# Performance work log

Measured on AMD Instinct MI355X. Metric: run time of the kernel, lower is better.

The kernel has to match this reference:

```python
import jax, jax.numpy as jnp
import numpy as np

D_MODEL = 1024
N_HEADS = 16
MAX_LAG = 512
D_K = D_MODEL // N_HEADS


def setup_inputs() -> dict:
    key = jax.random.key(0)
    ks = jax.random.split(key, 11)
    B, S = 2, 2048
    x = jax.random.normal(ks[0], (B, S, D_MODEL), dtype=jnp.float32)
    lag = jax.random.randint(ks[1], (S,), 0, MAX_LAG + 1, dtype=jnp.int64)
    scale = 1.0 / np.sqrt(D_MODEL)
    wq = jax.random.normal(ks[2], (D_MODEL, D_MODEL), dtype=jnp.float32) * scale
    bq = jnp.zeros((D_MODEL,), dtype=jnp.float32)
    wk = jax.random.normal(ks[3], (D_MODEL, D_MODEL), dtype=jnp.float32) * scale
    bk = jnp.zeros((D_MODEL,), dtype=jnp.float32)
    wv = jax.random.normal(ks[4], (D_MODEL, D_MODEL), dtype=jnp.float32) * scale
    bv = jnp.zeros((D_MODEL,), dtype=jnp.float32)
    wo = jax.random.normal(ks[5], (D_MODEL, D_MODEL), dtype=jnp.float32) * scale
    bo = jnp.zeros((D_MODEL,), dtype=jnp.float32)
    lag_bias = jax.random.normal(ks[6], (N_HEADS, MAX_LAG + 1), dtype=jnp.float32) * 0.02
    return {"x": x, "lag": lag, "wq": wq, "bq": bq, "wk": wk, "bk": bk,
            "wv": wv, "bv": bv, "wo": wo, "bo": bo, "lag_bias": lag_bias}


def reference(x, lag, wq, bq, wk, bk, wv, bv, wo, bo, lag_bias):
    B, S, D = x.shape
    H, dk = N_HEADS, D_K
    # projections: torch Linear is x @ W.T + b; here weights stored as (in, out)
    q = (x @ wq + bq).reshape(B, S, H, dk).transpose(0, 2, 1, 3)  # (B,H,S,dk)
    k = (x @ wk + bk).reshape(B, S, H, dk).transpose(0, 2, 1, 3)
    v = (x @ wv + bv).reshape(B, S, H, dk).transpose(0, 2, 1, 3)
    scores = jnp.einsum('bhqd,bhkd->bhqk', q, k) / jnp.sqrt(jnp.float32(dk))
    ld = jnp.abs(lag[:, None] - lag[None, :]).astype(jnp.int32)  # (S,S)
    bias = lag_bias[:, ld]  # (H,S,S)
    attn = jax.nn.softmax(scores + bias[None], axis=-1)
    out = jnp.einsum('bhqk,bhkd->bhqd', attn, v)
    out = out.transpose(0, 2, 1, 3).reshape(B, S, D)
    return out @ wo + bo
```

## Files before the change

### kernel.cpp

```cpp
#include <hip/hip_runtime.h>

typedef __bf16 bf16;
typedef __bf16 bf16x8 __attribute__((ext_vector_type(8)));
typedef float f32x4 __attribute__((ext_vector_type(4)));

__device__ __forceinline__ f32x4 mfma16(bf16x8 a, bf16x8 b, f32x4 c) {
  return __builtin_amdgcn_mfma_f32_16x16x32_bf16(a, b, c, 0, 0, 0);
}
__device__ __forceinline__ void gload16(const bf16* g, bf16* l) {
  __builtin_amdgcn_global_load_lds((const __attribute__((address_space(1))) unsigned int*)g,
                                   (__attribute__((address_space(3))) unsigned int*)l, 16, 0, 0);
}

__global__ __launch_bounds__(256) void cvt_x_kernel(const float* __restrict__ in,
                                                    bf16* __restrict__ out, int n8) {
  int i = blockIdx.x * 256 + threadIdx.x;
  if (i >= n8) return;
  const float4* p = (const float4*)in + (size_t)i * 2;
  float4 f0 = p[0], f1 = p[1];
  bf16x8 o;
  o[0] = (bf16)f0.x; o[1] = (bf16)f0.y; o[2] = (bf16)f0.z; o[3] = (bf16)f0.w;
  o[4] = (bf16)f1.x; o[5] = (bf16)f1.y; o[6] = (bf16)f1.z; o[7] = (bf16)f1.w;
  *((bf16x8*)out + i) = o;
}

__global__ __launch_bounds__(256) void cvt_wt_kernel(const float* __restrict__ in,
                                                     bf16* __restrict__ out) {
  __shared__ float t[64][68];
  int bx = blockIdx.x & 15;
  int by = blockIdx.x >> 4;
  int tid = threadIdx.x;
  int r = tid >> 2, p = tid & 3;
  const float* src = in + (size_t)(by * 64 + r) * 1024 + bx * 64 + p * 16;
#pragma unroll
  for (int j = 0; j < 16; j += 4)
    *(float4*)&t[r][p * 16 + j] = *(const float4*)(src + j);
  __syncthreads();
  int n = tid >> 2, sp = tid & 3;
  bf16 tmp[16];
#pragma unroll
  for (int j = 0; j < 16; ++j) tmp[j] = (bf16)t[sp * 16 + j][n];
  bf16* dst = out + (size_t)(bx * 64 + n) * 1024 + by * 64 + sp * 16;
  *(bf16x8*)dst = *(bf16x8*)&tmp[0];
  *(bf16x8*)(dst + 8) = *(bf16x8*)&tmp[8];
}

__global__ void cvt_bias_kernel(const float* __restrict__ bq, const float* __restrict__ bk,
                                const float* __restrict__ bv, float* __restrict__ out) {
  int i = blockIdx.x * 256 + threadIdx.x;
  if (i < 1024) out[i] = bq[i];
  else if (i < 2048) out[i] = bk[i - 1024];
  else if (i < 3072) out[i] = bv[i - 2048];
}

template <int OUT_BF16>
__global__ __launch_bounds__(256) void gemm_bt_kernel(
    const bf16* __restrict__ A, const bf16* __restrict__ Bt,
    const float* __restrict__ bias, void* __restrict__ C,
    int M, int N, int K, int scale_cols, float scale_val) {
  __shared__ __align__(16) bf16 As[128 * 64];
  __shared__ __align__(16) bf16 Bs[128 * 64];
  int bn = blockIdx.x * 128, bm = blockIdx.y * 128;
  int tid = threadIdx.x;
  int l = tid & 63;
  int w = tid >> 6;
  int wr = w >> 1, wc = w & 1;
  int g = l >> 4, c = l & 15;
  int swz = (c & 7) << 3;

  int srow = l >> 3;
  int scol = ((l & 7) ^ srow) << 3;
  const bf16* Ap = A + (size_t)(bm + w * 32 + srow) * K + scol;
  const bf16* Bp = Bt + (size_t)(bn + w * 32 + srow) * K + scol;
  bf16* AsW = As + w * 32 * 64;
  bf16* BsW = Bs + w * 32 * 64;

  f32x4 acc[4][4] = {};
  for (int k0 = 0; k0 < K; k0 += 64) {
    __syncthreads();
#pragma unroll
    for (int i = 0; i < 4; ++i) {
      gload16(Ap + (size_t)(8 * i) * K + k0, AsW + i * 512);
      gload16(Bp + (size_t)(8 * i) * K + k0, BsW + i * 512);
    }
    __syncthreads();
#pragma unroll
    for (int kh = 0; kh < 2; ++kh) {
      bf16x8 af[4], bfr[4];
#pragma unroll
      for (int m = 0; m < 4; ++m)
        af[m] = *(const bf16x8*)&As[(wr * 64 + m * 16 + c) * 64 + ((kh * 32 + g * 8) ^ swz)];
#pragma unroll
      for (int n = 0; n < 4; ++n)
        bfr[n] = *(const bf16x8*)&Bs[(wc * 64 + n * 16 + c) * 64 + ((kh * 32 + g * 8) ^ swz)];
#pragma unroll
      for (int m = 0; m < 4; ++m)
#pragma unroll
        for (int n = 0; n < 4; ++n)
          acc[m][n] = mfma16(af[m], bfr[n], acc[m][n]);
    }
  }
  int rowb = bm + wr * 64;
  int colb = bn + wc * 64;
#pragma unroll
  for (int n = 0; n < 4; ++n) {
    int col = colb + n * 16 + c;
    float bv = bias[col];
    float s = (col < scale_cols) ? scale_val : 1.0f;
#pragma unroll
    for (int m = 0; m < 4; ++m) {
      int row = rowb + m * 16 + g * 4;
#pragma unroll
      for (int j = 0; j < 4; ++j) {
        float v = (acc[m][n][j] + bv) * s;
        if (OUT_BF16)
          ((bf16*)C)[(size_t)(row + j) * N + col] = (bf16)v;
        else
          ((float*)C)[(size_t)(row + j) * N + col] = v;
      }
    }
  }
}

__global__ __launch_bounds__(256) void transpose_v_kernel(const bf16* __restrict__ qkv,
                                                          bf16* __restrict__ vt) {
  __shared__ bf16 t[64][72];
  int blk = blockIdx.x;
  int st = blk & 31;
  int h = (blk >> 5) & 15;
  int b = blk >> 9;
  int tid = threadIdx.x;
  int r = tid >> 2, p = tid & 3;
  const bf16* src = qkv + (size_t)(b * 2048 + st * 64 + r) * 3072 + 2048 + h * 64 + p * 16;
  *(bf16x8*)&t[r][p * 16] = *(const bf16x8*)src;
  *(bf16x8*)&t[r][p * 16 + 8] = *(const bf16x8*)(src + 8);
  __syncthreads();
  int d = tid >> 2, sp = tid & 3;
  bf16 tmp[16];
#pragma unroll
  for (int j = 0; j < 16; ++j) tmp[j] = t[sp * 16 + j][d];
  bf16* dst = vt + (size_t)((b * 16 + h) * 64 + d) * 2048 + st * 64 + sp * 16;
  *(bf16x8*)dst = *(bf16x8*)&tmp[0];
  *(bf16x8*)(dst + 8) = *(bf16x8*)&tmp[8];
}

__global__ __launch_bounds__(256) void attn_kernel(
    const bf16* __restrict__ qkv, const bf16* __restrict__ vt,
    const int* __restrict__ lag, const float* __restrict__ lag_bias,
    bf16* __restrict__ out) {
  __shared__ __align__(16) bf16 Ks0[64 * 64];
  __shared__ __align__(16) bf16 Vs0[64 * 64];
  __shared__ __align__(16) bf16 Ks1[64 * 64];
  __shared__ __align__(16) bf16 Vs1[64 * 64];
  __shared__ __align__(16) bf16 Ps[4][32][72];
  __shared__ float bias_s[516];
  __shared__ int lag_s[2048];

  int blk = blockIdx.x;
  blk = (blk & 7) * 64 + (blk >> 3);
  int qt = blk & 15;
  int h = (blk >> 4) & 15;
  int b = blk >> 8;
  int tid = threadIdx.x;
  int w = tid >> 6, l = tid & 63, g = l >> 4, c = l & 15;

  for (int i = tid; i < 513; i += 256) bias_s[i] = lag_bias[h * 513 + i] * 1.44269504f;
  for (int i = tid; i < 2048; i += 256) lag_s[i] = lag[i];

  int q0 = qt * 128 + w * 32;
  const bf16* qbase = qkv + (size_t)(b * 2048 + q0) * 3072 + h * 64;
  bf16x8 qf[2][2];
#pragma unroll
  for (int m = 0; m < 2; ++m)
#pragma unroll
    for (int kh = 0; kh < 2; ++kh)
      qf[m][kh] = *(const bf16x8*)(qbase + (size_t)(m * 16 + c) * 3072 + kh * 32 + g * 8);

  int swz = (c & 7) << 3;
  int off0 = (g * 8) ^ swz;
  int off1 = off0 ^ 32;

  int r0 = w * 16 + (l >> 3);
  int colE = ((l & 7) ^ (l >> 3)) << 3;
  const bf16* kbase = qkv + (size_t)(b * 2048) * 3072 + 1024 + h * 64;
  const bf16* vbase = vt + (size_t)(b * 16 + h) * 64 * 2048;
  const bf16* kg0 = kbase + (size_t)r0 * 3072 + colE;
  const bf16* kg1 = kbase + (size_t)(r0 + 8) * 3072 + colE;
  const bf16* vg0 = vbase + (size_t)r0 * 2048 + colE;
  const bf16* vg1 = vbase + (size_t)(r0 + 8) * 2048 + colE;

#define STAGE(KD, VD)                    \
  do {                                   \
    gload16(kg0, KD + w * 1024);         \
    gload16(kg1, KD + w * 1024 + 512);   \
    gload16(vg0, VD + w * 1024);         \
    gload16(vg1, VD + w * 1024 + 512);   \
    kg0 += 64 * 3072; kg1 += 64 * 3072;  \
    vg0 += 64; vg1 += 64;                \
  } while (0)

  STAGE(Ks0, Vs0);
  __syncthreads();

  int lagq[2][4];
#pragma unroll
  for (int m = 0; m < 2; ++m)
#pragma unroll
    for (int j = 0; j < 4; ++j) lagq[m][j] = lag_s[q0 + m * 16 + g * 4 + j];

  f32x4 oacc[2][4] = {};
  float psum[2][4] = {};

#define TILE(KB, VB, KT)                                                          \
  do {                                                                            \
    f32x4 sf[2][4] = {};                                                          \
    int lagk[4];                                                                  \
    __builtin_amdgcn_s_setprio(1);                                                \
    _Pragma("unroll") for (int kb = 0; kb < 4; ++kb) {                            \
      int row = kb * 16 + c;                                                      \
      bf16x8 k0 = *(const bf16x8*)&KB[row * 64 + off0];                           \
      bf16x8 k1 = *(const bf16x8*)&KB[row * 64 + off1];                           \
      sf[0][kb] = mfma16(qf[0][0], k0, sf[0][kb]);                                \
      sf[0][kb] = mfma16(qf[0][1], k1, sf[0][kb]);                                \
      sf[1][kb] = mfma16(qf[1][0], k0, sf[1][kb]);                                \
      sf[1][kb] = mfma16(qf[1][1], k1, sf[1][kb]);                                \
      lagk[kb] = lag_s[(KT) + kb * 16 + c];                                       \
    }                                                                             \
    __builtin_amdgcn_s_setprio(0);                                                \
    _Pragma("unroll") for (int m = 0; m < 2; ++m)                                 \
    _Pragma("unroll") for (int kb = 0; kb < 4; ++kb)                              \
    _Pragma("unroll") for (int j = 0; j < 4; ++j) {                               \
      int ld = lagq[m][j] - lagk[kb];                                             \
      ld = ld < 0 ? -ld : ld;                                                     \
      float p = __builtin_amdgcn_exp2f(sf[m][kb][j] + bias_s[ld]);                \
      psum[m][j] += p;                                                            \
      Ps[w][m * 16 + g * 4 + j][kb * 16 + c] = (bf16)p;                           \
    }                                                                             \
    asm volatile("s_waitcnt lgkmcnt(0)" ::: "memory");                            \
    __builtin_amdgcn_s_setprio(1);                                                \
    _Pragma("unroll") for (int ph = 0; ph < 2; ++ph) {                            \
      bf16x8 pa0 = *(const bf16x8*)&Ps[w][c][ph * 32 + g * 8];                    \
      bf16x8 pa1 = *(const bf16x8*)&Ps[w][16 + c][ph * 32 + g * 8];               \
      int voff = ph ? off1 : off0;                                                \
      _Pragma("unroll") for (int n = 0; n < 4; ++n) {                             \
        bf16x8 vf = *(const bf16x8*)&VB[(n * 16 + c) * 64 + voff];                \
        oacc[0][n] = mfma16(pa0, vf, oacc[0][n]);                                 \
        oacc[1][n] = mfma16(pa1, vf, oacc[1][n]);                                 \
      }                                                                           \
    }                                                                             \
    __builtin_amdgcn_s_setprio(0);                                                \
  } while (0)

  for (int kt = 0; kt < 2048; kt += 128) {
    if (kt + 64 < 2048) STAGE(Ks1, Vs1);
    TILE(Ks0, Vs0, kt);
    __syncthreads();
    if (kt + 128 < 2048) STAGE(Ks0, Vs0);
    TILE(Ks1, Vs1, kt + 64);
    __syncthreads();
  }

#pragma unroll
  for (int m = 0; m < 2; ++m) {
#pragma unroll
    for (int j = 0; j < 4; ++j) {
      float s = psum[m][j];
      s += __shfl_xor(s, 1);
      s += __shfl_xor(s, 2);
      s += __shfl_xor(s, 4);
      s += __shfl_xor(s, 8);
      float inv = 1.f / s;
      bf16* ob = out + (size_t)(b * 2048 + q0 + m * 16 + g * 4 + j) * 1024 + h * 64;
#pragma unroll
      for (int n = 0; n < 4; ++n)
        ob[n * 16 + c] = (bf16)(oacc[m][n][j] * inv);
    }
  }
#undef STAGE
#undef TILE
}

extern "C" void kernel_launch(void* const* d_in, const int* in_sizes, int n_in,
                              void* d_out, int out_size, void* d_ws, size_t ws_size,
                              hipStream_t stream) {
  const float* x        = (const float*)d_in[0];
  const int*   lag      = (const int*)d_in[1];
  const float* wq       = (const float*)d_in[2];
  const float* bq       = (const float*)d_in[3];
  const float* wk       = (const float*)d_in[4];
  const float* bk       = (const float*)d_in[5];
  const float* wv       = (const float*)d_in[6];
  const float* bv       = (const float*)d_in[7];
  const float* wo       = (const float*)d_in[8];
  const float* bo       = (const float*)d_in[9];
  const float* lag_bias = (const float*)d_in[10];

  char* ws = (char*)d_ws;
  bf16*  xb    = (bf16*)ws;
  bf16*  wqkvt = (bf16*)(ws + (8u  << 20));
  bf16*  wot   = (bf16*)(ws + (14u << 20));
  float* bqkv  = (float*)(ws + (16u << 20));
  bf16*  qkv   = (bf16*)(ws + (17u << 20));
  bf16*  vtb   = (bf16*)(ws + (41u << 20));
  bf16*  aout  = (bf16*)(ws + (49u << 20));

  cvt_x_kernel<<<2048, 256, 0, stream>>>(x, xb, 524288);
  cvt_wt_kernel<<<256, 256, 0, stream>>>(wq, wqkvt);
  cvt_wt_kernel<<<256, 256, 0, stream>>>(wk, wqkvt + (1u << 20));
  cvt_wt_kernel<<<256, 256, 0, stream>>>(wv, wqkvt + (2u << 20));
  cvt_wt_kernel<<<256, 256, 0, stream>>>(wo, wot);
  cvt_bias_kernel<<<12, 256, 0, stream>>>(bq, bk, bv, bqkv);
  gemm_bt_kernel<1><<<dim3(24, 32), 256, 0, stream>>>(
      xb, wqkvt, bqkv, qkv, 4096, 3072, 1024, 1024, 0.125f * 1.44269504f);
  transpose_v_kernel<<<1024, 256, 0, stream>>>(qkv, vtb);
  attn_kernel<<<512, 256, 0, stream>>>(qkv, vtb, lag, lag_bias, aout);
  gemm_bt_kernel<0><<<dim3(8, 32), 256, 0, stream>>>(
      aout, wot, bo, (float*)d_out, 4096, 1024, 1024, 0, 1.0f);
}
```

Measured before the change: 170.8 us.

## Permute keys by sorted lag and pack K contiguously for attention

Adds a single-block counting sort of the lag vector that produces a permutation and the sorted lag values. K is gathered in that order into a contiguous per-head buffer, and V is transposed in the same order, so attention reads K as dense 64-wide rows instead of 3072-strided rows. The sorted lags make bias lookups within a key tile more local. The sort runs on one block with a serial prefix and a scan per lag value, and the extra pack kernel adds a pass over K. The s_setprio hints inside the attention tile are also removed.

```diff
diff --git a/kernel.cpp b/kernel.cpp
--- a/kernel.cpp
+++ b/kernel.cpp
@@ -53,6 +53,45 @@
   else if (i < 3072) out[i] = bv[i - 2048];
 }
 
+__global__ __launch_bounds__(512) void sort_lag_kernel(const int* __restrict__ lag,
+                                                       int* __restrict__ perm,
+                                                       int* __restrict__ slag) {
+  __shared__ int l[2048];
+  __shared__ int cnt[513];
+  __shared__ int pre[513];
+  int tid = threadIdx.x;
+  for (int i = tid; i < 2048; i += 512) l[i] = lag[i];
+  for (int i = tid; i < 513; i += 512) cnt[i] = 0;
+  __syncthreads();
+  for (int i = tid; i < 2048; i += 512) atomicAdd(&cnt[l[i]], 1);
+  __syncthreads();
+  if (tid == 0) {
+    int a = 0;
+    for (int v = 0; v < 513; ++v) { pre[v] = a; a += cnt[v]; }
+  }
+  __syncthreads();
+  for (int v = tid; v < 513; v += 512) {
+    int base = pre[v];
+    for (int j = 0; j < 2048; ++j) {
+      if (l[j] == v) { perm[base] = j; slag[base] = v; ++base; }
+    }
+  }
+}
+
+__global__ __launch_bounds__(256) void pack_k_kernel(const bf16* __restrict__ qkv,
+                                                     const int* __restrict__ perm,
+                                                     bf16* __restrict__ kp) {
+  int blk = blockIdx.x;
+  int st = blk & 31, h = (blk >> 5) & 15, b = blk >> 9;
+  int tid = threadIdx.x;
+  int r = tid >> 2, p = tid & 3;
+  int src_s = perm[st * 64 + r];
+  const bf16* src = qkv + (size_t)(b * 2048 + src_s) * 3072 + 1024 + h * 64 + p * 16;
+  bf16* dst = kp + (size_t)((b * 16 + h) * 2048 + st * 64 + r) * 64 + p * 16;
+  *(bf16x8*)dst = *(const bf16x8*)src;
+  *(bf16x8*)(dst + 8) = *(const bf16x8*)(src + 8);
+}
+
 template <int OUT_BF16>
 __global__ __launch_bounds__(256) void gemm_bt_kernel(
     const bf16* __restrict__ A, const bf16* __restrict__ Bt,
@@ -123,6 +162,7 @@
 }
 
 __global__ __launch_bounds__(256) void transpose_v_kernel(const bf16* __restrict__ qkv,
+                                                          const int* __restrict__ perm,
                                                           bf16* __restrict__ vt) {
   __shared__ bf16 t[64][72];
   int blk = blockIdx.x;
@@ -131,7 +171,8 @@
   int b = blk >> 9;
   int tid = threadIdx.x;
   int r = tid >> 2, p = tid & 3;
-  const bf16* src = qkv + (size_t)(b * 2048 + st * 64 + r) * 3072 + 2048 + h * 64 + p * 16;
+  int src_s = perm[st * 64 + r];
+  const bf16* src = qkv + (size_t)(b * 2048 + src_s) * 3072 + 2048 + h * 64 + p * 16;
   *(bf16x8*)&t[r][p * 16] = *(const bf16x8*)src;
   *(bf16x8*)&t[r][p * 16 + 8] = *(const bf16x8*)(src + 8);
   __syncthreads();
@@ -145,8 +186,9 @@
 }
 
 __global__ __launch_bounds__(256) void attn_kernel(
-    const bf16* __restrict__ qkv, const bf16* __restrict__ vt,
-    const int* __restrict__ lag, const float* __restrict__ lag_bias,
+    const bf16* __restrict__ qkv, const bf16* __restrict__ kp,
+    const bf16* __restrict__ vt, const int* __restrict__ lag,
+    const int* __restrict__ slag, const float* __restrict__ lag_bias,
     bf16* __restrict__ out) {
   __shared__ __align__(16) bf16 Ks0[64 * 64];
   __shared__ __align__(16) bf16 Vs0[64 * 64];
@@ -165,7 +207,7 @@
   int w = tid >> 6, l = tid & 63, g = l >> 4, c = l & 15;
 
   for (int i = tid; i < 513; i += 256) bias_s[i] = lag_bias[h * 513 + i] * 1.44269504f;
-  for (int i = tid; i < 2048; i += 256) lag_s[i] = lag[i];
+  for (int i = tid; i < 2048; i += 256) lag_s[i] = slag[i];
 
   int q0 = qt * 128 + w * 32;
   const bf16* qbase = qkv + (size_t)(b * 2048 + q0) * 3072 + h * 64;
@@ -176,16 +218,22 @@
     for (int kh = 0; kh < 2; ++kh)
       qf[m][kh] = *(const bf16x8*)(qbase + (size_t)(m * 16 + c) * 3072 + kh * 32 + g * 8);
 
+  int lagq[2][4];
+#pragma unroll
+  for (int m = 0; m < 2; ++m)
+#pragma unroll
+    for (int j = 0; j < 4; ++j) lagq[m][j] = lag[q0 + m * 16 + g * 4 + j];
+
   int swz = (c & 7) << 3;
   int off0 = (g * 8) ^ swz;
   int off1 = off0 ^ 32;
 
   int r0 = w * 16 + (l >> 3);
   int colE = ((l & 7) ^ (l >> 3)) << 3;
-  const bf16* kbase = qkv + (size_t)(b * 2048) * 3072 + 1024 + h * 64;
+  const bf16* kbase = kp + (size_t)(b * 16 + h) * 2048 * 64;
   const bf16* vbase = vt + (size_t)(b * 16 + h) * 64 * 2048;
-  const bf16* kg0 = kbase + (size_t)r0 * 3072 + colE;
-  const bf16* kg1 = kbase + (size_t)(r0 + 8) * 3072 + colE;
+  const bf16* kg0 = kbase + (size_t)r0 * 64 + colE;
+  const bf16* kg1 = kbase + (size_t)(r0 + 8) * 64 + colE;
   const bf16* vg0 = vbase + (size_t)r0 * 2048 + colE;
   const bf16* vg1 = vbase + (size_t)(r0 + 8) * 2048 + colE;
 
@@ -195,18 +243,12 @@
     gload16(kg1, KD + w * 1024 + 512);   \
     gload16(vg0, VD + w * 1024);         \
     gload16(vg1, VD + w * 1024 + 512);   \
-    kg0 += 64 * 3072; kg1 += 64 * 3072;  \
+    kg0 += 64 * 64; kg1 += 64 * 64;      \
     vg0 += 64; vg1 += 64;                \
   } while (0)
 
   STAGE(Ks0, Vs0);
   __syncthreads();
-
-  int lagq[2][4];
-#pragma unroll
-  for (int m = 0; m < 2; ++m)
-#pragma unroll
-    for (int j = 0; j < 4; ++j) lagq[m][j] = lag_s[q0 + m * 16 + g * 4 + j];
 
   f32x4 oacc[2][4] = {};
   float psum[2][4] = {};
@@ -215,7 +257,6 @@
   do {                                                                            \
     f32x4 sf[2][4] = {};                                                          \
     int lagk[4];                                                                  \
-    __builtin_amdgcn_s_setprio(1);                                                \
     _Pragma("unroll") for (int kb = 0; kb < 4; ++kb) {                            \
       int row = kb * 16 + c;                                                      \
       bf16x8 k0 = *(const bf16x8*)&KB[row * 64 + off0];                           \
@@ -226,7 +267,6 @@
       sf[1][kb] = mfma16(qf[1][1], k1, sf[1][kb]);                                \
       lagk[kb] = lag_s[(KT) + kb * 16 + c];                                       \
     }                                                                             \
-    __builtin_amdgcn_s_setprio(0);                                                \
     _Pragma("unroll") for (int m = 0; m < 2; ++m)                                 \
     _Pragma("unroll") for (int kb = 0; kb < 4; ++kb)                              \
     _Pragma("unroll") for (int j = 0; j < 4; ++j) {                               \
@@ -237,7 +277,6 @@
       Ps[w][m * 16 + g * 4 + j][kb * 16 + c] = (bf16)p;                           \
     }                                                                             \
     asm volatile("s_waitcnt lgkmcnt(0)" ::: "memory");                            \
-    __builtin_amdgcn_s_setprio(1);                                                \
     _Pragma("unroll") for (int ph = 0; ph < 2; ++ph) {                            \
       bf16x8 pa0 = *(const bf16x8*)&Ps[w][c][ph * 32 + g * 8];                    \
       bf16x8 pa1 = *(const bf16x8*)&Ps[w][16 + c][ph * 32 + g * 8];               \
@@ -248,7 +287,6 @@
         oacc[1][n] = mfma16(pa1, vf, oacc[1][n]);                                 \
       }                                                                           \
     }                                                                             \
-    __builtin_amdgcn_s_setprio(0);                                                \
   } while (0)
 
   for (int kt = 0; kt < 2048; kt += 128) {
@@ -300,10 +338,14 @@
   bf16*  wqkvt = (bf16*)(ws + (8u  << 20));
   bf16*  wot   = (bf16*)(ws + (14u << 20));
   float* bqkv  = (float*)(ws + (16u << 20));
+  int*   perm  = (int*)(ws + (16u << 20) + 32768);
+  int*   slag  = (int*)(ws + (16u << 20) + 65536);
   bf16*  qkv   = (bf16*)(ws + (17u << 20));
   bf16*  vtb   = (bf16*)(ws + (41u << 20));
   bf16*  aout  = (bf16*)(ws + (49u << 20));
-
+  bf16*  kpk   = xb;
+
+  sort_lag_kernel<<<1, 512, 0, stream>>>(lag, perm, slag);
   cvt_x_kernel<<<2048, 256, 0, stream>>>(x, xb, 524288);
   cvt_wt_kernel<<<256, 256, 0, stream>>>(wq, wqkvt);
   cvt_wt_kernel<<<256, 256, 0, stream>>>(wk, wqkvt + (1u << 20));
@@ -312,8 +354,9 @@
   cvt_bias_kernel<<<12, 256, 0, stream>>>(bq, bk, bv, bqkv);
   gemm_bt_kernel<1><<<dim3(24, 32), 256, 0, stream>>>(
       xb, wqkvt, bqkv, qkv, 4096, 3072, 1024, 1024, 0.125f * 1.44269504f);
-  transpose_v_kernel<<<1024, 256, 0, stream>>>(qkv, vtb);
-  attn_kernel<<<512, 256, 0, stream>>>(qkv, vtb, lag, lag_bias, aout);
+  pack_k_kernel<<<1024, 256, 0, stream>>>(qkv, perm, kpk);
+  transpose_v_kernel<<<1024, 256, 0, stream>>>(qkv, perm, vtb);
+  attn_kernel<<<512, 256, 0, stream>>>(qkv, kpk, vtb, lag, slag, lag_bias, aout);
   gemm_bt_kernel<0><<<dim3(8, 32), 256, 0, stream>>>(
       aout, wot, bo, (float*)d_out, 4096, 1024, 1024, 0, 1.0f);
 }
```

Result: slower. 392.3 us (+129.7%).
